# Kernel optimization log

Hardware: AMD Instinct MI355X
Metric: run time of the kernel (lower is better)

The kernel has to match this reference:

```python
import jax, jax.numpy as jnp
import numpy as np

S = 3072      # total tokens across all images
DIM = 1280    # hidden_size
H = 16        # num_heads
HD = DIM // H # head_dim = 80
NSEG = 6      # number of images (cu_seqlens has NSEG+1 entries)


def _rotate_half(x):
    x1, x2 = jnp.split(x, 2, axis=-1)
    return jnp.concatenate([-x2, x1], axis=-1)


def setup_inputs() -> dict:
    key = jax.random.key(0)
    ks = jax.random.split(key, 12)
    hidden_states = jax.random.normal(ks[0], (S, DIM), jnp.float32)
    # realistic vision rotary embedding: half-dim inv_freq, repeated to head_dim
    inv_freq = 1.0 / (10000.0 ** (jnp.arange(0, HD // 2, dtype=jnp.float32) / (HD // 2)))
    freqs = jnp.arange(S, dtype=jnp.float32)[:, None] * inv_freq[None, :]  # [S, HD/2]
    emb = jnp.concatenate([freqs, freqs], axis=-1)  # [S, HD]
    cos = jnp.cos(emb)
    sin = jnp.sin(emb)
    sc = 0.02
    wq = jax.random.normal(ks[1], (DIM, DIM), jnp.float32) * sc
    bq = jax.random.normal(ks[2], (DIM,), jnp.float32) * sc
    wk = jax.random.normal(ks[3], (DIM, DIM), jnp.float32) * sc
    bk = jax.random.normal(ks[4], (DIM,), jnp.float32) * sc
    wv = jax.random.normal(ks[5], (DIM, DIM), jnp.float32) * sc
    bv = jax.random.normal(ks[6], (DIM,), jnp.float32) * sc
    wo = jax.random.normal(ks[7], (DIM, DIM), jnp.float32) * sc
    bo = jax.random.normal(ks[8], (DIM,), jnp.float32) * sc
    cu_seqlens = (jnp.arange(NSEG + 1, dtype=jnp.int32) * (S // NSEG))  # [0,512,...,3072]
    return dict(hidden_states=hidden_states, cos=cos, sin=sin,
                wq=wq, bq=bq, wk=wk, bk=bk, wv=wv, bv=bv, wo=wo, bo=bo,
                cu_seqlens=cu_seqlens)


def reference(hidden_states, cos, sin, wq, bq, wk, bk, wv, bv, wo, bo, cu_seqlens):
    seq_length = hidden_states.shape[0]
    scaling = HD ** (-0.5)
    # QKV projections (torch Linear: x @ W.T + b)
    q = (hidden_states @ wq.T + bq).reshape(seq_length, H, HD)
    k = (hidden_states @ wk.T + bk).reshape(seq_length, H, HD)
    v = (hidden_states @ wv.T + bv).reshape(seq_length, H, HD)
    # apply_rotary_pos_emb_vision: cos/sin [S, HD] broadcast over head axis
    c = cos[:, None, :]
    s = sin[:, None, :]
    q = q * c + _rotate_half(q) * s
    k = k * c + _rotate_half(k) * s
    # block-diagonal (per-image) attention via segment mask
    seg = jnp.searchsorted(cu_seqlens[1:], jnp.arange(seq_length), side='right')
    mask = seg[:, None] == seg[None, :]  # [S, S] bool
    scores = jnp.einsum('shd,thd->hst', q, k) * scaling  # [H, S, S]
    scores = jnp.where(mask[None, :, :], scores, jnp.finfo(scores.dtype).min)
    attn = jax.nn.softmax(scores, axis=-1)
    out = jnp.einsum('hst,thd->shd', attn, v).reshape(seq_length, DIM)
    return out @ wo.T + bo
```

## Files before the change

### kernel.cpp

```cpp
#include <hip/hip_runtime.h>
#include <hip/hip_bf16.h>
#include <hip/hip_fp16.h>
#include <cstdint>
#include <cstddef>

typedef _Float16 f16;
typedef f16 f16x2 __attribute__((ext_vector_type(2)));
typedef f16 f16x4 __attribute__((ext_vector_type(4)));
typedef f16 f16x8 __attribute__((ext_vector_type(8)));
typedef float f32x4 __attribute__((ext_vector_type(4)));

#define S_LEN 3072
#define DIM 1280
#define NH 16
#define HD 80
#define SEG 512

#define MFMA16F(a, b, c) __builtin_amdgcn_mfma_f32_16x16x32_f16((a), (b), (c), 0, 0, 0)

__device__ __forceinline__ void gl2lds16(const void* g, void* l) {
    __builtin_amdgcn_global_load_lds(
        (const __attribute__((address_space(1))) unsigned int*)g,
        (__attribute__((address_space(3))) unsigned int*)l, 16, 0, 0);
}

__device__ __forceinline__ unsigned int pack2(float a, float b) {
    f16x2 t = {(f16)a, (f16)b};
    union { f16x2 v; unsigned int u; } c;
    c.v = t;
    return c.u;
}

__global__ __launch_bounds__(256) void cvt_kernel(
    const float* __restrict__ hs,
    const float* __restrict__ wq, const float* __restrict__ wk,
    const float* __restrict__ wv, const float* __restrict__ wo,
    f16* __restrict__ hs16,
    f16* __restrict__ wq16, f16* __restrict__ wk16,
    f16* __restrict__ wv16, f16* __restrict__ wo16)
{
    const int m = blockIdx.y;
    const float* src; f16* dst; int n4;
    if (m == 0)      { src = hs; dst = hs16; n4 = S_LEN * DIM / 4; }
    else if (m == 1) { src = wq; dst = wq16; n4 = DIM * DIM / 4; }
    else if (m == 2) { src = wk; dst = wk16; n4 = DIM * DIM / 4; }
    else if (m == 3) { src = wv; dst = wv16; n4 = DIM * DIM / 4; }
    else             { src = wo; dst = wo16; n4 = DIM * DIM / 4; }
    int idx = blockIdx.x * 256 + threadIdx.x;
    if (idx >= n4) return;
    f32x4 v = *(const f32x4*)(src + (size_t)idx * 4);
    f16x4 o;
#pragma unroll
    for (int e = 0; e < 4; ++e) o[e] = (f16)v[e];
    *(f16x4*)(dst + (size_t)idx * 4) = o;
}

__global__ __launch_bounds__(512, 2) void gemm_qkv192(
    const f16* __restrict__ A, const f16* __restrict__ Wb,
    const float* __restrict__ bq, const float* __restrict__ bk,
    const float* __restrict__ bv,
    f16* __restrict__ q16, f16* __restrict__ k16, f16* __restrict__ vT)
{
    const int bid = blockIdx.x;
    const int xcd = bid & 7;
    const int idx = bid >> 3;
    const int mt = xcd * 2 + idx / 15;
    const int nt = idx % 15;
    const int m0 = mt * 192;
    const int n0 = nt * 256;

    __shared__ __align__(16) f16 Abuf[2][192 * 64];
    __shared__ __align__(16) f16 Bbuf[2][256 * 64];

    const int tid = threadIdx.x;
    const int w = tid >> 6;
    const int lane = tid & 63;
    const int lane15 = lane & 15;
    const int quad = lane >> 4;
    const int wm = (w >> 2) * 96;
    const int wn = (w & 3) * 64;

    const int srow = lane >> 3;
    const int schk = (lane & 7) ^ srow;

    const int aRow = w * 24;
    const int bRow = (w & 3) * 64 + (w >> 2) * 16;

    const f16* gA = A + (size_t)(m0 + aRow + srow) * DIM + schk * 8;
    const f16* gB = Wb + (size_t)(n0 + bRow + srow) * DIM + schk * 8;

    const int x7 = lane15 & 7;
    const int cc0 = (quad ^ x7) * 8;
    const int cc1 = ((quad + 4) ^ x7) * 8;

    f32x4 acc[6][4];
#pragma unroll
    for (int i = 0; i < 6; ++i)
#pragma unroll
        for (int j = 0; j < 4; ++j)
            acc[i][j] = (f32x4){0.f, 0.f, 0.f, 0.f};

    {
        f16* lA = Abuf[0] + aRow * 64;
        gl2lds16(gA, lA);
        gl2lds16(gA + 8 * DIM, lA + 512);
        gl2lds16(gA + 16 * DIM, lA + 1024);
        f16* lB = Bbuf[0] + bRow * 64;
        gl2lds16(gB, lB);
        gl2lds16(gB + 8 * DIM, lB + 512);
        gl2lds16(gB + 32 * DIM, lB + 2048);
        gl2lds16(gB + 40 * DIM, lB + 2560);
    }
    asm volatile("s_waitcnt vmcnt(0)" ::: "memory");
    __builtin_amdgcn_s_barrier();

    f16x8 a0[3][2], a1[3][2], b01a[2][2], b01b[2][2], b23[2][2];
#pragma unroll
    for (int j = 0; j < 2; ++j) {
        const f16* rp = Bbuf[0] + (wn + j * 16 + lane15) * 64;
        b01a[j][0] = *(const f16x8*)(rp + cc0);
        b01a[j][1] = *(const f16x8*)(rp + cc1);
    }
#pragma unroll
    for (int i = 0; i < 3; ++i) {
        const f16* rp = Abuf[0] + (wm + i * 16 + lane15) * 64;
        a0[i][0] = *(const f16x8*)(rp + cc0);
        a0[i][1] = *(const f16x8*)(rp + cc1);
    }

#pragma unroll 2
    for (int kt = 0; kt < 20; ++kt) {
        const int s = kt & 1;
        const int sn = s ^ 1;
        const int kn = (kt < 19) ? (kt + 1) : 19;
        const f16* As = Abuf[s];
        const f16* Bsl = Bbuf[s];
        const f16* Asn = Abuf[sn];
        const f16* Bsn = Bbuf[sn];
        const f16* gAn = gA + kn * 64;
        const f16* gBn = gB + kn * 64;

        {
            f16* lA = Abuf[sn] + aRow * 64;
            gl2lds16(gAn, lA);
            gl2lds16(gAn + 8 * DIM, lA + 512);
            gl2lds16(gAn + 16 * DIM, lA + 1024);
            f16* lB = Bbuf[sn] + bRow * 64;
            gl2lds16(gBn, lB);
            gl2lds16(gBn + 8 * DIM, lB + 512);
        }
#pragma unroll
        for (int j = 0; j < 2; ++j) {
            const f16* rp = Bsl + (wn + 32 + j * 16 + lane15) * 64;
            b23[j][0] = *(const f16x8*)(rp + cc0);
            b23[j][1] = *(const f16x8*)(rp + cc1);
        }
        __builtin_amdgcn_s_setprio(1);
#pragma unroll
        for (int i = 0; i < 3; ++i)
#pragma unroll
            for (int j = 0; j < 2; ++j) {
                acc[i][j] = MFMA16F(a0[i][0], b01a[j][0], acc[i][j]);
                acc[i][j] = MFMA16F(a0[i][1], b01a[j][1], acc[i][j]);
            }
        __builtin_amdgcn_s_setprio(0);
        __builtin_amdgcn_s_barrier();
        __builtin_amdgcn_sched_barrier(0);

        {
            f16* lB = Bbuf[sn] + bRow * 64 + 2048;
            gl2lds16(gBn + 32 * DIM, lB);
            gl2lds16(gBn + 40 * DIM, lB + 512);
        }
#pragma unroll
        for (int i = 0; i < 3; ++i) {
            const f16* rp = As + (wm + 48 + i * 16 + lane15) * 64;
            a1[i][0] = *(const f16x8*)(rp + cc0);
            a1[i][1] = *(const f16x8*)(rp + cc1);
        }
        __builtin_amdgcn_s_setprio(1);
#pragma unroll
        for (int i = 0; i < 3; ++i)
#pragma unroll
            for (int j = 0; j < 2; ++j) {
                acc[i][j + 2] = MFMA16F(a0[i][0], b23[j][0], acc[i][j + 2]);
                acc[i][j + 2] = MFMA16F(a0[i][1], b23[j][1], acc[i][j + 2]);
            }
        __builtin_amdgcn_s_setprio(0);
        __builtin_amdgcn_sched_barrier(0);

        asm volatile("s_waitcnt vmcnt(2)" ::: "memory");
        __builtin_amdgcn_s_barrier();
        __builtin_amdgcn_sched_barrier(0);
#pragma unroll
        for (int j = 0; j < 2; ++j) {
            const f16* rp = Bsn + (wn + j * 16 + lane15) * 64;
            b01b[j][0] = *(const f16x8*)(rp + cc0);
            b01b[j][1] = *(const f16x8*)(rp + cc1);
        }
        __builtin_amdgcn_s_setprio(1);
#pragma unroll
        for (int i = 0; i < 3; ++i)
#pragma unroll
            for (int j = 0; j < 2; ++j) {
                acc[i + 3][j + 2] = MFMA16F(a1[i][0], b23[j][0], acc[i + 3][j + 2]);
                acc[i + 3][j + 2] = MFMA16F(a1[i][1], b23[j][1], acc[i + 3][j + 2]);
            }
        __builtin_amdgcn_s_setprio(0);
        __builtin_amdgcn_sched_barrier(0);

#pragma unroll
        for (int i = 0; i < 3; ++i) {
            const f16* rp = Asn + (wm + i * 16 + lane15) * 64;
            a0[i][0] = *(const f16x8*)(rp + cc0);
            a0[i][1] = *(const f16x8*)(rp + cc1);
        }
        __builtin_amdgcn_s_setprio(1);
#pragma unroll
        for (int i = 0; i < 3; ++i)
#pragma unroll
            for (int j = 0; j < 2; ++j) {
                acc[i + 3][j] = MFMA16F(a1[i][0], b01a[j][0], acc[i + 3][j]);
                acc[i + 3][j] = MFMA16F(a1[i][1], b01a[j][1], acc[i + 3][j]);
            }
        __builtin_amdgcn_s_setprio(0);
#pragma unroll
        for (int j = 0; j < 2; ++j) {
            b01a[j][0] = b01b[j][0];
            b01a[j][1] = b01b[j][1];
        }
        asm volatile("s_waitcnt vmcnt(0)" ::: "memory");
        __builtin_amdgcn_s_barrier();
        __builtin_amdgcn_sched_barrier(0);
    }

    const int sel = nt / 5;
    const int nc0 = (nt % 5) * 256 + wn;
    const float* bias = (sel == 0) ? bq : (sel == 1) ? bk : bv;
    float bvv[4];
#pragma unroll
    for (int j = 0; j < 4; ++j) bvv[j] = bias[nc0 + j * 16 + lane15];

    if (sel < 2) {
        f16* O = sel ? k16 : q16;
#pragma unroll
        for (int i = 0; i < 6; ++i)
#pragma unroll
            for (int j = 0; j < 4; ++j)
#pragma unroll
                for (int r = 0; r < 4; ++r) {
                    int row = m0 + wm + i * 16 + quad * 4 + r;
                    O[(size_t)row * DIM + nc0 + j * 16 + lane15] =
                        (f16)(acc[i][j][r] + bvv[j]);
                }
    } else {
#pragma unroll
        for (int i = 0; i < 6; ++i)
#pragma unroll
            for (int j = 0; j < 4; ++j) {
                f16x4 ov;
#pragma unroll
                for (int r = 0; r < 4; ++r) ov[r] = (f16)(acc[i][j][r] + bvv[j]);
                int row = m0 + wm + i * 16 + quad * 4;
                int col = nc0 + j * 16 + lane15;
                *(f16x4*)(vT + (size_t)col * S_LEN + row) = ov;
            }
    }
}

__global__ __launch_bounds__(256) void gemm_out_kernel(
    const f16* __restrict__ A, const f16* __restrict__ W,
    const float* __restrict__ bias, float* __restrict__ OF)
{
    const int f = blockIdx.x;
    const int xcd = f & 7;
    const int idx = f >> 3;
    const int xt = xcd * 6 + idx % 6;
    const int yt = idx / 6;

    __shared__ __align__(16) f16 As[64 * 32];
    __shared__ __align__(16) f16 Bs[128 * 32];

    const int tid = threadIdx.x;
    const int lane = tid & 63;
    const int lane15 = tid & 15;
    const int quad = lane >> 4;
    const int w = tid >> 6;
    const int wn = w * 32;
    const int m0 = xt * 64;
    const int n0 = yt * 128;

    const int srA = w * 16 + (lane >> 2);
    const int srB = w * 32 + (lane >> 2);
    const int scol = (lane & 3) * 8;
    const f16* gA0 = A + (size_t)(m0 + srA) * DIM + scol;
    const f16* gB0 = W + (size_t)(n0 + srB) * DIM + scol;
    const f16* gB1 = W + (size_t)(n0 + srB + 16) * DIM + scol;
    f16* lA0 = As + (w * 16) * 32;
    f16* lB0 = Bs + (w * 32) * 32;
    f16* lB1 = Bs + (w * 32 + 16) * 32;

    f32x4 acc[4][2];
#pragma unroll
    for (int i = 0; i < 4; ++i)
#pragma unroll
        for (int j = 0; j < 2; ++j)
            acc[i][j] = (f32x4){0.f, 0.f, 0.f, 0.f};

    for (int kt = 0; kt < DIM / 32; ++kt) {
        __syncthreads();
        gl2lds16(gA0 + kt * 32, lA0);
        gl2lds16(gB0 + kt * 32, lB0);
        gl2lds16(gB1 + kt * 32, lB1);
        __syncthreads();

        f16x8 fa[4], fb[2];
#pragma unroll
        for (int i = 0; i < 4; ++i)
            fa[i] = *(const f16x8*)(As + (i * 16 + lane15) * 32 + quad * 8);
#pragma unroll
        for (int j = 0; j < 2; ++j)
            fb[j] = *(const f16x8*)(Bs + (wn + j * 16 + lane15) * 32 + quad * 8);
#pragma unroll
        for (int i = 0; i < 4; ++i)
#pragma unroll
            for (int j = 0; j < 2; ++j)
                acc[i][j] = MFMA16F(fa[i], fb[j], acc[i][j]);
    }

    float bvv[2];
#pragma unroll
    for (int j = 0; j < 2; ++j)
        bvv[j] = bias[n0 + wn + j * 16 + lane15];

#pragma unroll
    for (int i = 0; i < 4; ++i)
#pragma unroll
        for (int j = 0; j < 2; ++j)
#pragma unroll
            for (int r = 0; r < 4; ++r) {
                int row = m0 + i * 16 + quad * 4 + r;
                int col = n0 + wn + j * 16 + lane15;
                OF[(size_t)row * DIM + col] = acc[i][j][r] + bvv[j];
            }
}

__global__ __launch_bounds__(256) void rope_kernel(
    f16* __restrict__ qb, f16* __restrict__ kb,
    const float* __restrict__ cosb, const float* __restrict__ sinb)
{
    int idx = blockIdx.x * 256 + threadIdx.x;
    int c = idx % 5;
    int t = idx / 5;
    int h = t & 15; t >>= 4;
    int s = t % S_LEN;
    int which = t / S_LEN;
    f16* buf = which ? kb : qb;
    float scale = which ? 1.0f : 0.11180339887498948f;
    int j = c * 8;
    f32x4 ca = *(const f32x4*)(cosb + s * HD + j);
    f32x4 cb = *(const f32x4*)(cosb + s * HD + j + 4);
    f32x4 sna = *(const f32x4*)(sinb + s * HD + j);
    f32x4 snb = *(const f32x4*)(sinb + s * HD + j + 4);
    size_t base = (size_t)s * DIM + h * HD + j;
    f16x8 x1 = *(f16x8*)(buf + base);
    f16x8 x2 = *(f16x8*)(buf + base + 40);
    f16x8 o1, o2;
#pragma unroll
    for (int e = 0; e < 8; ++e) {
        float ce = (e < 4) ? ca[e] : cb[e - 4];
        float se = (e < 4) ? sna[e] : snb[e - 4];
        float a = (float)x1[e], b = (float)x2[e];
        o1[e] = (f16)((a * ce - b * se) * scale);
        o2[e] = (f16)((b * ce + a * se) * scale);
    }
    *(f16x8*)(buf + base) = o1;
    *(f16x8*)(buf + base + 40) = o2;
}

__global__ __launch_bounds__(256) void attn_kernel(
    const f16* __restrict__ q, const f16* __restrict__ k,
    const f16* __restrict__ vT, f16* __restrict__ o)
{
    const int h = blockIdx.x;
    const int g = blockIdx.y;
    const int qc = blockIdx.z;
    const int tid = threadIdx.x;
    const int lane15 = tid & 15;
    const int quad = (tid & 63) >> 4;
    const int w = tid >> 6;
    const int qbase = g * SEG + qc * 64;
    const int qrow = qbase + w * 16 + lane15;

    __shared__ __align__(16) f16 Ks[128 * 88];
    __shared__ __align__(16) f16 Vt[80 * 128];

    f16x8 zf;
#pragma unroll
    for (int e = 0; e < 8; ++e) zf[e] = (f16)0.0f;

    f16x8 fq[3];
#pragma unroll
    for (int kc = 0; kc < 3; ++kc) {
        if (kc == 2 && quad >= 2) fq[kc] = zf;
        else fq[kc] = *(const f16x8*)(q + (size_t)qrow * DIM + h * HD + kc * 32 + quad * 8);
    }

    float m_run = -1e30f, l_run = 0.f;
    f32x4 Oa[5];
#pragma unroll
    for (int dt = 0; dt < 5; ++dt) Oa[dt] = (f32x4){0.f, 0.f, 0.f, 0.f};

    for (int kt = 0; kt < 4; ++kt) {
        __syncthreads();
        const int kb = g * SEG + kt * 128;
#pragma unroll
        for (int c = tid; c < 1280; c += 256) {
            int r = c / 10;
            int c8 = (c - r * 10) * 8;
            *(f16x8*)(Ks + r * 88 + c8) =
                *(const f16x8*)(k + (size_t)(kb + r) * DIM + h * HD + c8);
        }
#pragma unroll
        for (int c = tid; c < 1280; c += 256) {
            int d = c >> 4;
            int sc = c & 15;
            *(f16x8*)(Vt + d * 128 + (sc ^ (d & 7)) * 8) =
                *(const f16x8*)(vT + (size_t)(h * HD + d) * S_LEN + kb + sc * 8);
        }
        __syncthreads();

        f32x4 sa[8];
#pragma unroll
        for (int nt = 0; nt < 8; ++nt) sa[nt] = (f32x4){0.f, 0.f, 0.f, 0.f};
#pragma unroll
        for (int kc = 0; kc < 3; ++kc) {
#pragma unroll
            for (int nt = 0; nt < 8; ++nt) {
                f16x8 fk;
                if (kc == 2 && quad >= 2) fk = zf;
                else fk = *(const f16x8*)(Ks + (nt * 16 + lane15) * 88 + kc * 32 + quad * 8);
                sa[nt] = MFMA16F(fk, fq[kc], sa[nt]);
            }
        }

        float mt = -1e30f;
#pragma unroll
        for (int nt = 0; nt < 8; ++nt)
#pragma unroll
            for (int r = 0; r < 4; ++r) mt = fmaxf(mt, sa[nt][r]);
        mt = fmaxf(mt, __shfl_xor(mt, 16, 64));
        mt = fmaxf(mt, __shfl_xor(mt, 32, 64));

        float mn = fmaxf(m_run, mt);
        float alpha = __expf(m_run - mn);
        m_run = mn;
        float lt = 0.f;
        unsigned int pp[8][2];
#pragma unroll
        for (int nt = 0; nt < 8; ++nt) {
            float p0 = __expf(sa[nt][0] - mn);
            float p1 = __expf(sa[nt][1] - mn);
            float p2 = __expf(sa[nt][2] - mn);
            float p3 = __expf(sa[nt][3] - mn);
            lt += (p0 + p1) + (p2 + p3);
            pp[nt][0] = pack2(p0, p1);
            pp[nt][1] = pack2(p2, p3);
        }
        lt += __shfl_xor(lt, 16, 64);
        lt += __shfl_xor(lt, 32, 64);
        l_run = l_run * alpha + lt;

#pragma unroll
        for (int dt = 0; dt < 5; ++dt)
#pragma unroll
            for (int r = 0; r < 4; ++r) Oa[dt][r] *= alpha;

        const int srcA = ((quad & 1) * 2) * 16 + lane15;
        const int srcB = srcA + 16;
        const bool hi = quad >= 2;
#pragma unroll
        for (int kc2 = 0; kc2 < 4; ++kc2) {
            unsigned int e0 = __shfl((int)pp[2 * kc2][0], srcA, 64);
            unsigned int e1 = __shfl((int)pp[2 * kc2][1], srcA, 64);
            unsigned int e2 = __shfl((int)pp[2 * kc2][0], srcB, 64);
            unsigned int e3 = __shfl((int)pp[2 * kc2][1], srcB, 64);
            unsigned int o0 = __shfl((int)pp[2 * kc2 + 1][0], srcA, 64);
            unsigned int o1 = __shfl((int)pp[2 * kc2 + 1][1], srcA, 64);
            unsigned int o2 = __shfl((int)pp[2 * kc2 + 1][0], srcB, 64);
            unsigned int o3 = __shfl((int)pp[2 * kc2 + 1][1], srcB, 64);
            union { unsigned int u[4]; f16x8 v; } fp;
            fp.u[0] = hi ? o0 : e0;
            fp.u[1] = hi ? o1 : e1;
            fp.u[2] = hi ? o2 : e2;
            fp.u[3] = hi ? o3 : e3;
#pragma unroll
            for (int dt = 0; dt < 5; ++dt) {
                int drow = dt * 16 + lane15;
                int slot = (kc2 * 4 + quad) ^ (drow & 7);
                f16x8 fv = *(const f16x8*)(Vt + drow * 128 + slot * 8);
                Oa[dt] = MFMA16F(fv, fp.v, Oa[dt]);
            }
        }
    }

    float inv = 1.0f / l_run;
#pragma unroll
    for (int dt = 0; dt < 5; ++dt) {
        f16x4 ov;
#pragma unroll
        for (int r = 0; r < 4; ++r) ov[r] = (f16)(Oa[dt][r] * inv);
        *(f16x4*)(o + (size_t)qrow * DIM + h * HD + dt * 16 + quad * 4) = ov;
    }
}

extern "C" void kernel_launch(void* const* d_in, const int* in_sizes, int n_in,
                              void* d_out, int out_size, void* d_ws, size_t ws_size,
                              hipStream_t stream)
{
    const float* hs   = (const float*)d_in[0];
    const float* cosb = (const float*)d_in[1];
    const float* sinb = (const float*)d_in[2];
    const float* wq   = (const float*)d_in[3];
    const float* bq   = (const float*)d_in[4];
    const float* wk   = (const float*)d_in[5];
    const float* bk   = (const float*)d_in[6];
    const float* wv   = (const float*)d_in[7];
    const float* bv   = (const float*)d_in[8];
    const float* wo   = (const float*)d_in[9];
    const float* bo   = (const float*)d_in[10];

    const size_t SD = (size_t)S_LEN * DIM;
    const size_t WW = (size_t)DIM * DIM;
    f16* hs16 = (f16*)d_ws;
    f16* wq16 = hs16 + SD;
    f16* wk16 = wq16 + WW;
    f16* wv16 = wk16 + WW;
    f16* wo16 = wv16 + WW;
    f16* q16  = wo16 + WW;
    f16* k16  = q16 + SD;
    f16* vT16 = k16 + SD;
    f16* ao16 = vT16 + SD;
    float* outb = (float*)d_out;

    cvt_kernel<<<dim3(S_LEN * DIM / 4 / 256, 5), 256, 0, stream>>>(
        hs, wq, wk, wv, wo, hs16, wq16, wk16, wv16, wo16);
    gemm_qkv192<<<240, 512, 0, stream>>>(
        hs16, wq16, bq, bk, bv, q16, k16, vT16);
    rope_kernel<<<1920, 256, 0, stream>>>(q16, k16, cosb, sinb);
    attn_kernel<<<dim3(NH, 6, 8), 256, 0, stream>>>(q16, k16, vT16, ao16);
    gemm_out_kernel<<<480, 256, 0, stream>>>(ao16, wo16, bo, outb);
}
```

Baseline: 217.9 us.

## Fuse fp32-to-fp16 conversion into QKV GEMM and RoPE into attention

The QKV GEMM now reads fp32 hidden states and weights directly, converting them to fp16 in registers before writing to LDS, rather than using global_load_lds on pre-converted buffers. This removes the separate conversion pass over hidden states and three weight matrices, and only wo is still converted up front. The standalone RoPE kernel is removed and the rotation is applied inside the attention kernel when loading Q fragments and K tiles. In exchange the GEMM reads twice the bytes per tile and loses the direct-to-LDS path. Attention now recomputes RoPE on K for every query chunk, 8 times per key tile, with extra cos/sin loads.

```diff
diff --git a/kernel.cpp b/kernel.cpp
--- a/kernel.cpp
+++ b/kernel.cpp
@@ -17,6 +17,7 @@
 #define SEG 512
 
 #define MFMA16F(a, b, c) __builtin_amdgcn_mfma_f32_16x16x32_f16((a), (b), (c), 0, 0, 0)
+#define LD4(p) (*(const f32x4*)(p))
 
 __device__ __forceinline__ void gl2lds16(const void* g, void* l) {
     __builtin_amdgcn_global_load_lds(
@@ -31,32 +32,28 @@
     return c.u;
 }
 
-__global__ __launch_bounds__(256) void cvt_kernel(
+__device__ __forceinline__ f16x8 cvt8(f32x4 lo, f32x4 hi) {
+    f16x8 o;
+#pragma unroll
+    for (int e = 0; e < 4; ++e) { o[e] = (f16)lo[e]; o[e + 4] = (f16)hi[e]; }
+    return o;
+}
+
+__global__ __launch_bounds__(256) void cvt_wo_kernel(
+    const float* __restrict__ wo, f16* __restrict__ wo16)
+{
+    int idx = blockIdx.x * 256 + threadIdx.x;
+    f32x4 v = *(const f32x4*)(wo + (size_t)idx * 4);
+    f16x4 o;
+#pragma unroll
+    for (int e = 0; e < 4; ++e) o[e] = (f16)v[e];
+    *(f16x4*)(wo16 + (size_t)idx * 4) = o;
+}
+
+__global__ __launch_bounds__(512, 2) void gemm_qkv192(
     const float* __restrict__ hs,
     const float* __restrict__ wq, const float* __restrict__ wk,
-    const float* __restrict__ wv, const float* __restrict__ wo,
-    f16* __restrict__ hs16,
-    f16* __restrict__ wq16, f16* __restrict__ wk16,
-    f16* __restrict__ wv16, f16* __restrict__ wo16)
-{
-    const int m = blockIdx.y;
-    const float* src; f16* dst; int n4;
-    if (m == 0)      { src = hs; dst = hs16; n4 = S_LEN * DIM / 4; }
-    else if (m == 1) { src = wq; dst = wq16; n4 = DIM * DIM / 4; }
-    else if (m == 2) { src = wk; dst = wk16; n4 = DIM * DIM / 4; }
-    else if (m == 3) { src = wv; dst = wv16; n4 = DIM * DIM / 4; }
-    else             { src = wo; dst = wo16; n4 = DIM * DIM / 4; }
-    int idx = blockIdx.x * 256 + threadIdx.x;
-    if (idx >= n4) return;
-    f32x4 v = *(const f32x4*)(src + (size_t)idx * 4);
-    f16x4 o;
-#pragma unroll
-    for (int e = 0; e < 4; ++e) o[e] = (f16)v[e];
-    *(f16x4*)(dst + (size_t)idx * 4) = o;
-}
-
-__global__ __launch_bounds__(512, 2) void gemm_qkv192(
-    const f16* __restrict__ A, const f16* __restrict__ Wb,
+    const float* __restrict__ wv,
     const float* __restrict__ bq, const float* __restrict__ bk,
     const float* __restrict__ bv,
     f16* __restrict__ q16, f16* __restrict__ k16, f16* __restrict__ vT)
@@ -67,7 +64,10 @@
     const int mt = xcd * 2 + idx / 15;
     const int nt = idx % 15;
     const int m0 = mt * 192;
-    const int n0 = nt * 256;
+
+    const int sel = nt / 5;
+    const float* Wsel = (sel == 0) ? wq : (sel == 1) ? wk : wv;
+    const int bn0 = (nt % 5) * 256;
 
     __shared__ __align__(16) f16 Abuf[2][192 * 64];
     __shared__ __align__(16) f16 Bbuf[2][256 * 64];
@@ -86,8 +86,8 @@
     const int aRow = w * 24;
     const int bRow = (w & 3) * 64 + (w >> 2) * 16;
 
-    const f16* gA = A + (size_t)(m0 + aRow + srow) * DIM + schk * 8;
-    const f16* gB = Wb + (size_t)(n0 + bRow + srow) * DIM + schk * 8;
+    const float* gA = hs + (size_t)(m0 + aRow + srow) * DIM + schk * 8;
+    const float* gB = Wsel + (size_t)(bn0 + bRow + srow) * DIM + schk * 8;
 
     const int x7 = lane15 & 7;
     const int cc0 = (quad ^ x7) * 8;
@@ -100,18 +100,27 @@
         for (int j = 0; j < 4; ++j)
             acc[i][j] = (f32x4){0.f, 0.f, 0.f, 0.f};
 
+    f32x4 la[6], lbf[4], lbs[4];
+
+    la[0] = LD4(gA);             la[1] = LD4(gA + 4);
+    la[2] = LD4(gA + 8 * DIM);   la[3] = LD4(gA + 8 * DIM + 4);
+    la[4] = LD4(gA + 16 * DIM);  la[5] = LD4(gA + 16 * DIM + 4);
+    lbf[0] = LD4(gB);            lbf[1] = LD4(gB + 4);
+    lbf[2] = LD4(gB + 8 * DIM);  lbf[3] = LD4(gB + 8 * DIM + 4);
+    lbs[0] = LD4(gB + 32 * DIM); lbs[1] = LD4(gB + 32 * DIM + 4);
+    lbs[2] = LD4(gB + 40 * DIM); lbs[3] = LD4(gB + 40 * DIM + 4);
     {
-        f16* lA = Abuf[0] + aRow * 64;
-        gl2lds16(gA, lA);
-        gl2lds16(gA + 8 * DIM, lA + 512);
-        gl2lds16(gA + 16 * DIM, lA + 1024);
-        f16* lB = Bbuf[0] + bRow * 64;
-        gl2lds16(gB, lB);
-        gl2lds16(gB + 8 * DIM, lB + 512);
-        gl2lds16(gB + 32 * DIM, lB + 2048);
-        gl2lds16(gB + 40 * DIM, lB + 2560);
-    }
-    asm volatile("s_waitcnt vmcnt(0)" ::: "memory");
+        f16* wA = Abuf[0] + aRow * 64 + lane * 8;
+        *(f16x8*)(wA)        = cvt8(la[0], la[1]);
+        *(f16x8*)(wA + 512)  = cvt8(la[2], la[3]);
+        *(f16x8*)(wA + 1024) = cvt8(la[4], la[5]);
+        f16* wB = Bbuf[0] + bRow * 64 + lane * 8;
+        *(f16x8*)(wB)        = cvt8(lbf[0], lbf[1]);
+        *(f16x8*)(wB + 512)  = cvt8(lbf[2], lbf[3]);
+        *(f16x8*)(wB + 2048) = cvt8(lbs[0], lbs[1]);
+        *(f16x8*)(wB + 2560) = cvt8(lbs[2], lbs[3]);
+    }
+    asm volatile("s_waitcnt lgkmcnt(0)" ::: "memory");
     __builtin_amdgcn_s_barrier();
 
     f16x8 a0[3][2], a1[3][2], b01a[2][2], b01b[2][2], b23[2][2];
@@ -128,27 +137,23 @@
         a0[i][1] = *(const f16x8*)(rp + cc1);
     }
 
-#pragma unroll 2
     for (int kt = 0; kt < 20; ++kt) {
         const int s = kt & 1;
-        const int sn = s ^ 1;
+        const int snx = s ^ 1;
         const int kn = (kt < 19) ? (kt + 1) : 19;
         const f16* As = Abuf[s];
         const f16* Bsl = Bbuf[s];
-        const f16* Asn = Abuf[sn];
-        const f16* Bsn = Bbuf[sn];
-        const f16* gAn = gA + kn * 64;
-        const f16* gBn = gB + kn * 64;
-
-        {
-            f16* lA = Abuf[sn] + aRow * 64;
-            gl2lds16(gAn, lA);
-            gl2lds16(gAn + 8 * DIM, lA + 512);
-            gl2lds16(gAn + 16 * DIM, lA + 1024);
-            f16* lB = Bbuf[sn] + bRow * 64;
-            gl2lds16(gBn, lB);
-            gl2lds16(gBn + 8 * DIM, lB + 512);
-        }
+        const f16* Asn = Abuf[snx];
+        const f16* Bsn = Bbuf[snx];
+        const float* gAn = gA + kn * 64;
+        const float* gBn = gB + kn * 64;
+
+        la[0] = LD4(gAn);             la[1] = LD4(gAn + 4);
+        la[2] = LD4(gAn + 8 * DIM);   la[3] = LD4(gAn + 8 * DIM + 4);
+        la[4] = LD4(gAn + 16 * DIM);  la[5] = LD4(gAn + 16 * DIM + 4);
+        lbf[0] = LD4(gBn);            lbf[1] = LD4(gBn + 4);
+        lbf[2] = LD4(gBn + 8 * DIM);  lbf[3] = LD4(gBn + 8 * DIM + 4);
+        __builtin_amdgcn_sched_barrier(0);
 #pragma unroll
         for (int j = 0; j < 2; ++j) {
             const f16* rp = Bsl + (wn + 32 + j * 16 + lane15) * 64;
@@ -164,14 +169,11 @@
                 acc[i][j] = MFMA16F(a0[i][1], b01a[j][1], acc[i][j]);
             }
         __builtin_amdgcn_s_setprio(0);
-        __builtin_amdgcn_s_barrier();
         __builtin_amdgcn_sched_barrier(0);
 
-        {
-            f16* lB = Bbuf[sn] + bRow * 64 + 2048;
-            gl2lds16(gBn + 32 * DIM, lB);
-            gl2lds16(gBn + 40 * DIM, lB + 512);
-        }
+        lbs[0] = LD4(gBn + 32 * DIM); lbs[1] = LD4(gBn + 32 * DIM + 4);
+        lbs[2] = LD4(gBn + 40 * DIM); lbs[3] = LD4(gBn + 40 * DIM + 4);
+        __builtin_amdgcn_sched_barrier(0);
 #pragma unroll
         for (int i = 0; i < 3; ++i) {
             const f16* rp = As + (wm + 48 + i * 16 + lane15) * 64;
@@ -187,11 +189,23 @@
                 acc[i][j + 2] = MFMA16F(a0[i][1], b23[j][1], acc[i][j + 2]);
             }
         __builtin_amdgcn_s_setprio(0);
-        __builtin_amdgcn_sched_barrier(0);
-
-        asm volatile("s_waitcnt vmcnt(2)" ::: "memory");
+        asm volatile("s_waitcnt vmcnt(8)" ::: "memory");
+        {
+            f16* wA = Abuf[snx] + aRow * 64 + lane * 8;
+            *(f16x8*)(wA)        = cvt8(la[0], la[1]);
+            *(f16x8*)(wA + 512)  = cvt8(la[2], la[3]);
+            *(f16x8*)(wA + 1024) = cvt8(la[4], la[5]);
+        }
+        asm volatile("s_waitcnt vmcnt(4)" ::: "memory");
+        {
+            f16* wB = Bbuf[snx] + bRow * 64 + lane * 8;
+            *(f16x8*)(wB)       = cvt8(lbf[0], lbf[1]);
+            *(f16x8*)(wB + 512) = cvt8(lbf[2], lbf[3]);
+        }
+        asm volatile("s_waitcnt lgkmcnt(0)" ::: "memory");
         __builtin_amdgcn_s_barrier();
         __builtin_amdgcn_sched_barrier(0);
+
 #pragma unroll
         for (int j = 0; j < 2; ++j) {
             const f16* rp = Bsn + (wn + j * 16 + lane15) * 64;
@@ -224,17 +238,22 @@
                 acc[i + 3][j] = MFMA16F(a1[i][1], b01a[j][1], acc[i + 3][j]);
             }
         __builtin_amdgcn_s_setprio(0);
+        asm volatile("s_waitcnt vmcnt(0)" ::: "memory");
+        {
+            f16* wS = Bbuf[snx] + bRow * 64 + 2048 + lane * 8;
+            *(f16x8*)(wS)       = cvt8(lbs[0], lbs[1]);
+            *(f16x8*)(wS + 512) = cvt8(lbs[2], lbs[3]);
+        }
 #pragma unroll
         for (int j = 0; j < 2; ++j) {
             b01a[j][0] = b01b[j][0];
             b01a[j][1] = b01b[j][1];
         }
-        asm volatile("s_waitcnt vmcnt(0)" ::: "memory");
+        asm volatile("s_waitcnt lgkmcnt(0)" ::: "memory");
         __builtin_amdgcn_s_barrier();
         __builtin_amdgcn_sched_barrier(0);
     }
 
-    const int sel = nt / 5;
     const int nc0 = (nt % 5) * 256 + wn;
     const float* bias = (sel == 0) ? bq : (sel == 1) ? bk : bv;
     float bvv[4];
@@ -345,42 +364,11 @@
             }
 }
 
-__global__ __launch_bounds__(256) void rope_kernel(
-    f16* __restrict__ qb, f16* __restrict__ kb,
-    const float* __restrict__ cosb, const float* __restrict__ sinb)
-{
-    int idx = blockIdx.x * 256 + threadIdx.x;
-    int c = idx % 5;
-    int t = idx / 5;
-    int h = t & 15; t >>= 4;
-    int s = t % S_LEN;
-    int which = t / S_LEN;
-    f16* buf = which ? kb : qb;
-    float scale = which ? 1.0f : 0.11180339887498948f;
-    int j = c * 8;
-    f32x4 ca = *(const f32x4*)(cosb + s * HD + j);
-    f32x4 cb = *(const f32x4*)(cosb + s * HD + j + 4);
-    f32x4 sna = *(const f32x4*)(sinb + s * HD + j);
-    f32x4 snb = *(const f32x4*)(sinb + s * HD + j + 4);
-    size_t base = (size_t)s * DIM + h * HD + j;
-    f16x8 x1 = *(f16x8*)(buf + base);
-    f16x8 x2 = *(f16x8*)(buf + base + 40);
-    f16x8 o1, o2;
-#pragma unroll
-    for (int e = 0; e < 8; ++e) {
-        float ce = (e < 4) ? ca[e] : cb[e - 4];
-        float se = (e < 4) ? sna[e] : snb[e - 4];
-        float a = (float)x1[e], b = (float)x2[e];
-        o1[e] = (f16)((a * ce - b * se) * scale);
-        o2[e] = (f16)((b * ce + a * se) * scale);
-    }
-    *(f16x8*)(buf + base) = o1;
-    *(f16x8*)(buf + base + 40) = o2;
-}
-
 __global__ __launch_bounds__(256) void attn_kernel(
     const f16* __restrict__ q, const f16* __restrict__ k,
-    const f16* __restrict__ vT, f16* __restrict__ o)
+    const f16* __restrict__ vT,
+    const float* __restrict__ cosb, const float* __restrict__ sinb,
+    f16* __restrict__ o)
 {
     const int h = blockIdx.x;
     const int g = blockIdx.y;
@@ -399,11 +387,31 @@
 #pragma unroll
     for (int e = 0; e < 8; ++e) zf[e] = (f16)0.0f;
 
+    const f16* qr = q + (size_t)qrow * DIM + h * HD;
+    const float* cq = cosb + (size_t)qrow * HD;
+    const float* sq = sinb + (size_t)qrow * HD;
     f16x8 fq[3];
 #pragma unroll
     for (int kc = 0; kc < 3; ++kc) {
-        if (kc == 2 && quad >= 2) fq[kc] = zf;
-        else fq[kc] = *(const f16x8*)(q + (size_t)qrow * DIM + h * HD + kc * 32 + quad * 8);
+        if (kc == 2 && quad >= 2) { fq[kc] = zf; }
+        else {
+            const int c = kc * 32 + quad * 8;
+            const int p = (c < 40) ? c + 40 : c - 40;
+            const float sgn = (c < 40) ? -1.f : 1.f;
+            f16x8 xc = *(const f16x8*)(qr + c);
+            f16x8 xp = *(const f16x8*)(qr + p);
+            f32x4 c0 = LD4(cq + c), c1 = LD4(cq + c + 4);
+            f32x4 s0 = LD4(sq + c), s1 = LD4(sq + c + 4);
+            f16x8 ov;
+#pragma unroll
+            for (int e = 0; e < 8; ++e) {
+                float ce = (e < 4) ? c0[e] : c1[e - 4];
+                float se = (e < 4) ? s0[e] : s1[e - 4];
+                ov[e] = (f16)((((float)xc[e]) * ce + sgn * ((float)xp[e]) * se)
+                              * 0.11180339887498948f);
+            }
+            fq[kc] = ov;
+        }
     }
 
     float m_run = -1e30f, l_run = 0.f;
@@ -418,8 +426,23 @@
         for (int c = tid; c < 1280; c += 256) {
             int r = c / 10;
             int c8 = (c - r * 10) * 8;
-            *(f16x8*)(Ks + r * 88 + c8) =
-                *(const f16x8*)(k + (size_t)(kb + r) * DIM + h * HD + c8);
+            int p8 = (c8 < 40) ? c8 + 40 : c8 - 40;
+            float sgn = (c8 < 40) ? -1.f : 1.f;
+            const f16* kr = k + (size_t)(kb + r) * DIM + h * HD;
+            f16x8 xc = *(const f16x8*)(kr + c8);
+            f16x8 xp = *(const f16x8*)(kr + p8);
+            const float* ck = cosb + (size_t)(kb + r) * HD + c8;
+            const float* sk = sinb + (size_t)(kb + r) * HD + c8;
+            f32x4 c0 = LD4(ck), c1 = LD4(ck + 4);
+            f32x4 s0 = LD4(sk), s1 = LD4(sk + 4);
+            f16x8 ov;
+#pragma unroll
+            for (int e = 0; e < 8; ++e) {
+                float ce = (e < 4) ? c0[e] : c1[e - 4];
+                float se = (e < 4) ? s0[e] : s1[e - 4];
+                ov[e] = (f16)(((float)xc[e]) * ce + sgn * ((float)xp[e]) * se);
+            }
+            *(f16x8*)(Ks + r * 88 + c8) = ov;
         }
 #pragma unroll
         for (int c = tid; c < 1280; c += 256) {
@@ -532,22 +555,17 @@
 
     const size_t SD = (size_t)S_LEN * DIM;
     const size_t WW = (size_t)DIM * DIM;
-    f16* hs16 = (f16*)d_ws;
-    f16* wq16 = hs16 + SD;
-    f16* wk16 = wq16 + WW;
-    f16* wv16 = wk16 + WW;
-    f16* wo16 = wv16 + WW;
-    f16* q16  = wo16 + WW;
+    f16* q16  = (f16*)d_ws;
     f16* k16  = q16 + SD;
     f16* vT16 = k16 + SD;
     f16* ao16 = vT16 + SD;
+    f16* wo16 = ao16 + SD;
     float* outb = (float*)d_out;
 
-    cvt_kernel<<<dim3(S_LEN * DIM / 4 / 256, 5), 256, 0, stream>>>(
-        hs, wq, wk, wv, wo, hs16, wq16, wk16, wv16, wo16);
+    cvt_wo_kernel<<<DIM * DIM / 4 / 256, 256, 0, stream>>>(wo, wo16);
     gemm_qkv192<<<240, 512, 0, stream>>>(
-        hs16, wq16, bq, bk, bv, q16, k16, vT16);
-    rope_kernel<<<1920, 256, 0, stream>>>(q16, k16, cosb, sinb);
-    attn_kernel<<<dim3(NH, 6, 8), 256, 0, stream>>>(q16, k16, vT16, ao16);
+        hs, wq, wk, wv, bq, bk, bv, q16, k16, vT16);
+    attn_kernel<<<dim3(NH, 6, 8), 256, 0, stream>>>(
+        q16, k16, vT16, cosb, sinb, ao16);
     gemm_out_kernel<<<480, 256, 0, stream>>>(ao16, wo16, bo, outb);
 }
```

New measurement: 251.3 us. +15.3%, slower.
